# Kernel optimization log

Measured on AMD Instinct MI355X. Metric: run time of the kernel, lower is better.

The kernel has to match this reference:

```python
import jax, jax.numpy as jnp
import numpy as np

N_NODES = 100000
N_EDGES = 1600000
F_IN = 128
H = 32
N_CLASSES = 2
N_GRAPHS = 1000
BN_EPS = 1e-5


def _glorot(key, shape):
    fan_in, fan_out = shape
    lim = float(np.sqrt(6.0 / (fan_in + fan_out)))
    return jax.random.uniform(key, shape, jnp.float32, -lim, lim)


def setup_inputs() -> dict:
    key = jax.random.key(0)
    ks = jax.random.split(key, 16)
    x = jax.random.normal(ks[0], (N_NODES, F_IN), jnp.float32)
    edge_index = jax.random.randint(ks[1], (2, N_EDGES), 0, N_NODES, jnp.int64)
    batch = jnp.sort(jax.random.randint(ks[2], (N_NODES,), 0, N_GRAPHS, jnp.int64))
    return {
        "x": x,
        "edge_index": edge_index,
        "batch": batch,
        # GIN layer 1 MLP: Linear(F_IN,H) -> BN(H) -> ReLU -> Linear(H,H)
        "W1": _glorot(ks[3], (F_IN, H)), "b1": jnp.zeros((H,), jnp.float32),
        "g1": jnp.ones((H,), jnp.float32), "be1": jnp.zeros((H,), jnp.float32),
        "W2": _glorot(ks[4], (H, H)), "b2": jnp.zeros((H,), jnp.float32),
        # GIN layer 2 MLP
        "W3": _glorot(ks[5], (H, H)), "b3": jnp.zeros((H,), jnp.float32),
        "g2": jnp.ones((H,), jnp.float32), "be2": jnp.zeros((H,), jnp.float32),
        "W4": _glorot(ks[6], (H, H)), "b4": jnp.zeros((H,), jnp.float32),
        # classifier: Linear(2H,H) -> ReLU -> (Dropout eval) -> Linear(H,C)
        "Wc1": _glorot(ks[7], (2 * H, H)), "bc1": jnp.zeros((H,), jnp.float32),
        "Wc2": _glorot(ks[8], (H, N_CLASSES)), "bc2": jnp.zeros((N_CLASSES,), jnp.float32),
    }


def _gin_conv(x, src, dst, W_a, b_a, g, be, W_b, b_b):
    # GIN aggregation with eps=0: (1+eps)*x + sum_{j in N(i)} x_j
    agg = x + jax.ops.segment_sum(x[src], dst, num_segments=N_NODES)
    h = agg @ W_a + b_a                    # [N, H]
    # BatchNorm1d over node dim (training-mode batch stats)
    mu = jnp.mean(h, axis=0)
    var = jnp.var(h, axis=0)
    h = (h - mu) * jax.lax.rsqrt(var + BN_EPS) * g + be
    h = jax.nn.relu(h)
    return h @ W_b + b_b                   # [N, H]


def reference(x, edge_index, batch,
              W1, b1, g1, be1, W2, b2,
              W3, b3, g2, be2, W4, b4,
              Wc1, bc1, Wc2, bc2):
    src, dst = edge_index[0], edge_index[1]
    h = jax.nn.relu(_gin_conv(x, src, dst, W1, b1, g1, be1, W2, b2))
    h = _gin_conv(h, src, dst, W3, b3, g2, be2, W4, b4)   # [N, H]
    # global mean + max pool per graph
    counts = jax.ops.segment_sum(jnp.ones((N_NODES,), h.dtype), batch,
                                 num_segments=N_GRAPHS)              # [G]
    sums = jax.ops.segment_sum(h, batch, num_segments=N_GRAPHS)      # [G, H]
    mean = sums / jnp.maximum(counts, 1.0)[:, None]
    mx = jax.ops.segment_max(h, batch, num_segments=N_GRAPHS)
    mx = jnp.where(counts[:, None] > 0, mx, 0.0)
    z = jnp.concatenate([mean, mx], axis=-1)                          # [G, 2H]
    z = jax.nn.relu(z @ Wc1 + bc1)                                    # dropout: eval mode (identity)
    return z @ Wc2 + bc2                                              # [G, C]
```

## Files before the change

### kernel.cpp

```cpp
#include <hip/hip_runtime.h>


#define H 32
#define FIN 128
#define AGG_BLOCKS 2048
#define BNRED_NB 64

#define BKT_SHIFT 9
#define BKT_SZ 512
#define ACHUNK 4096

__device__ __forceinline__ int lower_bound_i(const int* __restrict__ a, int n, int key) {
  int lo = 0, hi = n;
  while (lo < hi) { int mid = (lo + hi) >> 1; if (a[mid] < key) lo = mid + 1; else hi = mid; }
  return lo;
}


__global__ __launch_bounds__(256) void k_bhist(const int* __restrict__ dst, int E,
                                               int* __restrict__ gbcnt) {
  __shared__ int cnt[256];
  int t = threadIdx.x;
  int e0 = blockIdx.x * ACHUNK, e1 = min(e0 + ACHUNK, E);
  cnt[t] = 0;
  __syncthreads();
  for (int i = e0 + t; i < e1; i += 256) atomicAdd(&cnt[dst[i] >> BKT_SHIFT], 1);
  __syncthreads();
  if (cnt[t] > 0) atomicAdd(&gbcnt[t], cnt[t]);
}

__global__ __launch_bounds__(256) void k_bscan(const int* __restrict__ gbcnt, int nbuck,
                                               int* __restrict__ bbase, int* __restrict__ bcur) {
  int t = threadIdx.x;
  __shared__ int sh[256];
  int v0 = (t < nbuck) ? gbcnt[t] : 0;
  sh[t] = v0;
  __syncthreads();
  for (int d = 1; d < 256; d <<= 1) {
    int v = (t >= d) ? sh[t - d] : 0;
    __syncthreads();
    sh[t] += v;
    __syncthreads();
  }
  int excl = sh[t] - v0;
  if (t < nbuck) { bbase[t] = excl; bcur[t] = excl; }
  if (t == 255) bbase[nbuck] = sh[255];
}

__global__ __launch_bounds__(256) void k_bucketA(const int* __restrict__ src, const int* __restrict__ dst,
                                                 int E, int* __restrict__ bcur,
                                                 unsigned* __restrict__ staging) {
  __shared__ int cnt[256];
  __shared__ int base[256];
  int t = threadIdx.x;
  int e0 = blockIdx.x * ACHUNK, e1 = min(e0 + ACHUNK, E);
  cnt[t] = 0;
  __syncthreads();
  for (int i = e0 + t; i < e1; i += 256) atomicAdd(&cnt[dst[i] >> BKT_SHIFT], 1);
  __syncthreads();
  int c = cnt[t];
  base[t] = (c > 0) ? atomicAdd(&bcur[t], c) : 0;
  __syncthreads();
  for (int i = e0 + t; i < e1; i += 256) {
    int d = dst[i];
    int p = atomicAdd(&base[d >> BKT_SHIFT], 1);
    staging[p] = ((unsigned)(d & (BKT_SZ - 1)) << 17) | (unsigned)src[i];
  }
}

__global__ __launch_bounds__(256) void k_bucketB(const unsigned* __restrict__ staging,
                                                 const int* __restrict__ bbase, int N,
                                                 int* __restrict__ row_ptr, int* __restrict__ csr) {
  __shared__ int cnt[BKT_SZ];
  __shared__ int ptr[BKT_SZ];
  __shared__ int sc[256];
  int t = threadIdx.x, b = blockIdx.x;
  int nb0 = b << BKT_SHIFT;
  int nb1 = min(nb0 + BKT_SZ, N);
  int seg0 = bbase[b];
  int len = bbase[b + 1] - seg0;
  cnt[t] = 0; cnt[t + 256] = 0;
  __syncthreads();
  for (int i = t; i < len; i += 256) atomicAdd(&cnt[staging[seg0 + i] >> 17], 1);
  __syncthreads();
  int s2 = cnt[2 * t] + cnt[2 * t + 1];
  sc[t] = s2;
  __syncthreads();
  for (int d = 1; d < 256; d <<= 1) {
    int v = (t >= d) ? sc[t - d] : 0;
    __syncthreads();
    sc[t] += v;
    __syncthreads();
  }
  int base0 = sc[t] - s2;
  ptr[2 * t] = base0;
  ptr[2 * t + 1] = base0 + cnt[2 * t];
  __syncthreads();
  int nn = nb1 - nb0;
  if (2 * t < nn)     row_ptr[nb0 + 2 * t]     = seg0 + ptr[2 * t];
  if (2 * t + 1 < nn) row_ptr[nb0 + 2 * t + 1] = seg0 + ptr[2 * t + 1];
  if (t == 0 && nb1 == N) row_ptr[N] = seg0 + len;
  __syncthreads();
  for (int i = t; i < len; i += 256) {
    unsigned e = staging[seg0 + i];
    int d = (int)(e >> 17);
    int k = atomicAdd(&ptr[d], 1);
    csr[seg0 + k] = (int)(e & 0x1FFFFu);
  }
}


__global__ __launch_bounds__(256) void k_gemm1(const float* __restrict__ x, const float* __restrict__ W,
                                               float* __restrict__ y, int N) {
  __shared__ __align__(16) float ws[FIN * H];
  __shared__ __align__(16) float xs[128 * 33];
  int t = threadIdx.x;
  for (int i = t; i < FIN * H; i += 256) ws[i] = W[i];
  int nb = blockIdx.x * 128;
  int r0 = (t >> 3) * 4;
  int c0 = (t & 7) * 4;
  float acc[4][4] = {{0.f,0.f,0.f,0.f},{0.f,0.f,0.f,0.f},{0.f,0.f,0.f,0.f},{0.f,0.f,0.f,0.f}};
  for (int kb = 0; kb < FIN; kb += 32) {
    __syncthreads();
    for (int i = t; i < 1024; i += 256) {
      int n = i >> 3, k4 = (i & 7) * 4;
      float4 v = make_float4(0.f, 0.f, 0.f, 0.f);
      int gn = nb + n;
      if (gn < N) v = *(const float4*)&x[(size_t)gn * FIN + kb + k4];
      xs[n * 33 + k4 + 0] = v.x; xs[n * 33 + k4 + 1] = v.y;
      xs[n * 33 + k4 + 2] = v.z; xs[n * 33 + k4 + 3] = v.w;
    }
    __syncthreads();
#pragma unroll
    for (int k = 0; k < 32; ++k) {
      float4 wv = *(const float4*)&ws[(kb + k) * H + c0];
      float x0 = xs[(r0 + 0) * 33 + k];
      float x1 = xs[(r0 + 1) * 33 + k];
      float x2 = xs[(r0 + 2) * 33 + k];
      float x3 = xs[(r0 + 3) * 33 + k];
      acc[0][0] += x0 * wv.x; acc[0][1] += x0 * wv.y; acc[0][2] += x0 * wv.z; acc[0][3] += x0 * wv.w;
      acc[1][0] += x1 * wv.x; acc[1][1] += x1 * wv.y; acc[1][2] += x1 * wv.z; acc[1][3] += x1 * wv.w;
      acc[2][0] += x2 * wv.x; acc[2][1] += x2 * wv.y; acc[2][2] += x2 * wv.z; acc[2][3] += x2 * wv.w;
      acc[3][0] += x3 * wv.x; acc[3][1] += x3 * wv.y; acc[3][2] += x3 * wv.z; acc[3][3] += x3 * wv.w;
    }
  }
#pragma unroll
  for (int r = 0; r < 4; ++r) {
    int gn = nb + r0 + r;
    if (gn < N)
      *(float4*)&y[(size_t)gn * H + c0] = make_float4(acc[r][0], acc[r][1], acc[r][2], acc[r][3]);
  }
}

__global__ __launch_bounds__(256) void k_agg(const float* __restrict__ y, const float* __restrict__ bias,
                                             const int* __restrict__ row_ptr, const int* __restrict__ csr,
                                             float* __restrict__ hout, float* __restrict__ bn_part, int N) {
  int wid = threadIdx.x >> 6, lane = threadIdx.x & 63;
  int c = lane & 31, ep = lane >> 5;
  float rsum = 0.f, rsq = 0.f;
  float bc = bias[c];
  int stride = gridDim.x * 4;
  for (int n = blockIdx.x * 4 + wid; n < N; n += stride) {
    int beg = row_ptr[n], end = row_ptr[n + 1];
    float acc = 0.f;
    for (int b0 = beg; b0 < end; b0 += 64) {
      int m = end - b0; if (m > 64) m = 64;
      int idx = (lane < m) ? csr[b0 + lane] : 0;
      int r = 0;
      for (; r + 8 <= m; r += 8) {
        int j0 = __shfl(idx, r + 0 + ep, 64);
        int j1 = __shfl(idx, r + 2 + ep, 64);
        int j2 = __shfl(idx, r + 4 + ep, 64);
        int j3 = __shfl(idx, r + 6 + ep, 64);
        float v0 = y[(size_t)j0 * H + c];
        float v1 = y[(size_t)j1 * H + c];
        float v2 = y[(size_t)j2 * H + c];
        float v3 = y[(size_t)j3 * H + c];
        acc += (v0 + v1) + (v2 + v3);
      }
      for (; r < m; r += 2) {
        int s = r + ep;
        int j = __shfl(idx, (s < m) ? s : 0, 64);
        float val = y[(size_t)j * H + c];
        if (s < m) acc += val;
      }
    }
    acc += __shfl_xor(acc, 32, 64);
    float v = acc + y[(size_t)n * H + c] + bc;
    if (ep == 0) {
      hout[(size_t)n * H + c] = v;
      rsum += v; rsq += v * v;
    }
  }
  __shared__ float bsum[4][H], bsq[4][H];
  if (ep == 0) { bsum[wid][c] = rsum; bsq[wid][c] = rsq; }
  __syncthreads();
  if (threadIdx.x < H) {
    int cc = threadIdx.x;
    bn_part[(size_t)blockIdx.x * 64 + cc]     = bsum[0][cc] + bsum[1][cc] + bsum[2][cc] + bsum[3][cc];
    bn_part[(size_t)blockIdx.x * 64 + H + cc] = bsq[0][cc] + bsq[1][cc] + bsq[2][cc] + bsq[3][cc];
  }
}

__global__ __launch_bounds__(256) void k_bnred(const float* __restrict__ part,
                                               float* __restrict__ part2) {
  int t = threadIdx.x, b = blockIdx.x;
  int col = t & 63, q = t >> 6;
  int rpb = AGG_BLOCKS / BNRED_NB;
  int r0 = b * rpb + q * (rpb / 4);
  float s = 0.f;
  for (int r = r0; r < r0 + rpb / 4; ++r) s += part[(size_t)r * 64 + col];
  __shared__ float red[4][64];
  red[q][col] = s;
  __syncthreads();
  if (t < 64) part2[(size_t)b * 64 + t] = red[0][t] + red[1][t] + red[2][t] + red[3][t];
}

__global__ __launch_bounds__(256) void k_bnfin(const float* __restrict__ part, int nblk,
                                               const float* __restrict__ gma, const float* __restrict__ bet,
                                               float* __restrict__ sc, float invN) {
  int t = threadIdx.x;
  int col = t & 63, q = t >> 6;
  int per = nblk >> 2;
  float s = 0.f;
  for (int r = q * per; r < (q + 1) * per; ++r) s += part[(size_t)r * 64 + col];
  __shared__ float red[4][64];
  __shared__ float tot[64];
  red[q][col] = s;
  __syncthreads();
  if (t < 64) tot[t] = red[0][t] + red[1][t] + red[2][t] + red[3][t];
  __syncthreads();
  if (t < H) {
    float mean = tot[t] * invN;
    float var = tot[H + t] * invN - mean * mean;
    float scale = gma[t] * rsqrtf(var + 1e-5f);
    sc[t] = scale;
    sc[H + t] = bet[t] - mean * scale;
  }
}

__global__ __launch_bounds__(256) void k_mlp1(const float* __restrict__ h1, const float* __restrict__ sc,
                                              const float* __restrict__ W2, const float* __restrict__ b2,
                                              const float* __restrict__ W3, float* __restrict__ y2, int N) {
  __shared__ __align__(16) float ws2[H * H], ws3[H * H];
  int t = threadIdx.x;
  for (int i = t; i < H * H; i += 256) { ws2[i] = W2[i]; ws3[i] = W3[i]; }
  __syncthreads();
  int lane = t & 63, wid = t >> 6;
  int c = lane & 31;
  int n = (blockIdx.x * 4 + wid) * 2 + (lane >> 5);
  if (n >= N) return;
  float h = h1[(size_t)n * H + c];
  float a = fmaxf(h * sc[c] + sc[H + c], 0.f);
  float u = b2[c];
#pragma unroll
  for (int k = 0; k < H; ++k)
    u += __shfl(a, k, 32) * ws2[k * H + c];
  u = fmaxf(u, 0.f);
  float o = 0.f;
#pragma unroll
  for (int k = 0; k < H; ++k)
    o += __shfl(u, k, 32) * ws3[k * H + c];
  y2[(size_t)n * H + c] = o;
}

__global__ __launch_bounds__(256) void k_mlp2(const float* __restrict__ hpre, const float* __restrict__ sc,
                                              const float* __restrict__ W4, const float* __restrict__ b4,
                                              float* __restrict__ h2, int N) {
  __shared__ __align__(16) float ws4[H * H];
  int t = threadIdx.x;
  for (int i = t; i < H * H; i += 256) ws4[i] = W4[i];
  __syncthreads();
  int lane = t & 63, wid = t >> 6;
  int c = lane & 31;
  int n = (blockIdx.x * 4 + wid) * 2 + (lane >> 5);
  if (n >= N) return;
  float h = hpre[(size_t)n * H + c];
  float a = fmaxf(h * sc[c] + sc[H + c], 0.f);
  float o = b4[c];
#pragma unroll
  for (int k = 0; k < H; ++k)
    o += __shfl(a, k, 32) * ws4[k * H + c];
  h2[(size_t)n * H + c] = o;
}

__global__ __launch_bounds__(256) void k_pool(const float* __restrict__ h2, const int* __restrict__ batch,
                                              int N, int G, float* __restrict__ z) {
  int wid = threadIdx.x >> 6, lane = threadIdx.x & 63;
  int g = blockIdx.x * 4 + wid;
  if (g >= G) return;
  int beg = lower_bound_i(batch, N, g);
  int end = lower_bound_i(batch, N, g + 1);
  int c = lane & 31, ep = lane >> 5;
  float s = 0.f, m = -3.402823466e38f;
  for (int i = beg + ep; i < end; i += 2) {
    float v = h2[(size_t)i * H + c];
    s += v; m = fmaxf(m, v);
  }
  s += __shfl_xor(s, 32, 64);
  m = fmaxf(m, __shfl_xor(m, 32, 64));
  if (ep == 0) {
    int cnt = end - beg;
    z[(size_t)g * 64 + c]     = (cnt > 0) ? s / (float)cnt : 0.f;
    z[(size_t)g * 64 + H + c] = (cnt > 0) ? m : 0.f;
  }
}

__global__ __launch_bounds__(256) void k_cls(const float* __restrict__ z, const float* __restrict__ Wc1,
                                             const float* __restrict__ bc1, const float* __restrict__ Wc2,
                                             const float* __restrict__ bc2, float* __restrict__ out, int G) {
  __shared__ __align__(16) float w1s[64 * H];
  __shared__ float w2s[H * 2], b1s[H], b2s[2];
  int t = threadIdx.x;
  for (int i = t; i < 64 * H; i += 256) w1s[i] = Wc1[i];
  if (t < H * 2) w2s[t] = Wc2[t];
  if (t < H) b1s[t] = bc1[t];
  if (t < 2) b2s[t] = bc2[t];
  __syncthreads();
  int g = blockIdx.x * 256 + t;
  if (g >= G) return;
  float zr[64], u[H];
  const float4* zp = (const float4*)&z[(size_t)g * 64];
#pragma unroll
  for (int q = 0; q < 16; ++q) {
    float4 v = zp[q];
    zr[q * 4 + 0] = v.x; zr[q * 4 + 1] = v.y; zr[q * 4 + 2] = v.z; zr[q * 4 + 3] = v.w;
  }
#pragma unroll
  for (int c = 0; c < H; ++c) u[c] = b1s[c];
#pragma unroll
  for (int k = 0; k < 64; ++k) {
    float av = zr[k];
    const float4* wr = (const float4*)&w1s[k * H];
#pragma unroll
    for (int q = 0; q < H / 4; ++q) {
      float4 wv = wr[q];
      u[q * 4 + 0] += av * wv.x; u[q * 4 + 1] += av * wv.y;
      u[q * 4 + 2] += av * wv.z; u[q * 4 + 3] += av * wv.w;
    }
  }
  float o0 = b2s[0], o1 = b2s[1];
#pragma unroll
  for (int k = 0; k < H; ++k) {
    float uv = fmaxf(u[k], 0.f);
    o0 += uv * w2s[k * 2 + 0];
    o1 += uv * w2s[k * 2 + 1];
  }
  out[(size_t)g * 2 + 0] = o0;
  out[(size_t)g * 2 + 1] = o1;
}

extern "C" void kernel_launch(void* const* d_in, const int* in_sizes, int n_in,
                              void* d_out, int out_size, void* d_ws, size_t ws_size,
                              hipStream_t stream) {
  const float* x    = (const float*)d_in[0];
  const int*   eidx = (const int*)d_in[1];
  const int*   batch= (const int*)d_in[2];
  const float* W1 = (const float*)d_in[3];
  const float* b1 = (const float*)d_in[4];
  const float* g1 = (const float*)d_in[5];
  const float* be1= (const float*)d_in[6];
  const float* W2 = (const float*)d_in[7];
  const float* b2 = (const float*)d_in[8];
  const float* W3 = (const float*)d_in[9];
  const float* b3 = (const float*)d_in[10];
  const float* g2 = (const float*)d_in[11];
  const float* be2= (const float*)d_in[12];
  const float* W4 = (const float*)d_in[13];
  const float* b4 = (const float*)d_in[14];
  const float* Wc1= (const float*)d_in[15];
  const float* bc1= (const float*)d_in[16];
  const float* Wc2= (const float*)d_in[17];
  const float* bc2= (const float*)d_in[18];
  (void)n_in; (void)ws_size;

  int N = in_sizes[2];
  int E = in_sizes[1] / 2;
  int G = out_size / 2;
  int nbuck = (N + BKT_SZ - 1) >> BKT_SHIFT;
  const int* srcv = eidx;
  const int* dstv = eidx + E;

  char* w = (char*)d_ws;
  auto carve = [&](size_t bytes) { void* p = (void*)w; w += (bytes + 255) & ~(size_t)255; return p; };
  float*    bufA    = (float*)carve((size_t)N * H * 4);
  float*    bufB    = (float*)carve((size_t)N * H * 4);
  int*      row_ptr = (int*)carve((size_t)(N + 1) * 4);
  int*      csr     = (int*)carve((size_t)E * 4);
  unsigned* staging = (unsigned*)carve((size_t)E * 4);
  int*      gbcnt   = (int*)carve(256 * 4);
  int*      bbase   = (int*)carve(257 * 4);
  int*      bcur    = (int*)carve(256 * 4);
  float*    bnp     = (float*)carve((size_t)AGG_BLOCKS * 64 * 4);
  float*    bnp2    = (float*)carve((size_t)BNRED_NB * 64 * 4);
  float*    sc1     = (float*)carve(64 * 4);
  float*    sc2     = (float*)carve(64 * 4);
  float*    z       = (float*)carve((size_t)G * 64 * 4);

  int abk = (E + ACHUNK - 1) / ACHUNK;
  int mlpblk = ((N + 1) / 2 + 3) / 4;

  hipMemsetAsync(gbcnt, 0, 256 * 4, stream);
  k_bhist<<<abk, 256, 0, stream>>>(dstv, E, gbcnt);
  k_bscan<<<1, 256, 0, stream>>>(gbcnt, nbuck, bbase, bcur);
  k_bucketA<<<abk, 256, 0, stream>>>(srcv, dstv, E, bcur, staging);
  k_bucketB<<<nbuck, 256, 0, stream>>>(staging, bbase, N, row_ptr, csr);
  k_gemm1<<<(N + 127) / 128, 256, 0, stream>>>(x, W1, bufA, N);
  k_agg<<<AGG_BLOCKS, 256, 0, stream>>>(bufA, b1, row_ptr, csr, bufB, bnp, N);
  k_bnred<<<BNRED_NB, 256, 0, stream>>>(bnp, bnp2);
  k_bnfin<<<1, 256, 0, stream>>>(bnp2, BNRED_NB, g1, be1, sc1, 1.0f / (float)N);
  k_mlp1<<<mlpblk, 256, 0, stream>>>(bufB, sc1, W2, b2, W3, bufA, N);
  k_agg<<<AGG_BLOCKS, 256, 0, stream>>>(bufA, b3, row_ptr, csr, bufB, bnp, N);
  k_bnred<<<BNRED_NB, 256, 0, stream>>>(bnp, bnp2);
  k_bnfin<<<1, 256, 0, stream>>>(bnp2, BNRED_NB, g2, be2, sc2, 1.0f / (float)N);
  k_mlp2<<<mlpblk, 256, 0, stream>>>(bufB, sc2, W4, b4, bufA, N);
  k_pool<<<(G + 3) / 4, 256, 0, stream>>>(bufA, batch, N, G, z);
  k_cls<<<(G + 255) / 256, 256, 0, stream>>>(z, Wc1, bc1, Wc2, bc2, (float*)d_out, G);
}
```

Baseline: 413.8 us.

## Tile the per-node MLP kernels as 128-node register-blocked GEMMs in shared memory

k_mlp1 and k_mlp2 now stage a 128-node tile of activations in padded shared memory. Each thread computes a 4x4 register block using float4 weight loads, instead of one output per lane built from 32 shuffles. The goal is to cut shuffle and LDS instruction overhead and to use vectorized global loads and stores. The cost is more shared memory per block, which may lower occupancy, and extra barriers.

New measurement: 389.6 us. 5.9% less time.

```diff
diff --git a/kernel.cpp b/kernel.cpp
--- a/kernel.cpp
+++ b/kernel.cpp
@@ -243,45 +243,123 @@
                                               const float* __restrict__ W2, const float* __restrict__ b2,
                                               const float* __restrict__ W3, float* __restrict__ y2, int N) {
   __shared__ __align__(16) float ws2[H * H], ws3[H * H];
+  __shared__ __align__(16) float as[128 * 33];
+  __shared__ __align__(16) float us[128 * 33];
+  __shared__ float scs[2 * H], b2s[H];
   int t = threadIdx.x;
   for (int i = t; i < H * H; i += 256) { ws2[i] = W2[i]; ws3[i] = W3[i]; }
-  __syncthreads();
-  int lane = t & 63, wid = t >> 6;
-  int c = lane & 31;
-  int n = (blockIdx.x * 4 + wid) * 2 + (lane >> 5);
-  if (n >= N) return;
-  float h = h1[(size_t)n * H + c];
-  float a = fmaxf(h * sc[c] + sc[H + c], 0.f);
-  float u = b2[c];
-#pragma unroll
-  for (int k = 0; k < H; ++k)
-    u += __shfl(a, k, 32) * ws2[k * H + c];
-  u = fmaxf(u, 0.f);
-  float o = 0.f;
-#pragma unroll
-  for (int k = 0; k < H; ++k)
-    o += __shfl(u, k, 32) * ws3[k * H + c];
-  y2[(size_t)n * H + c] = o;
+  if (t < 2 * H) scs[t] = sc[t];
+  if (t < H) b2s[t] = b2[t];
+  __syncthreads();
+  int nb = blockIdx.x * 128;
+  for (int i = t; i < 1024; i += 256) {
+    int n = i >> 3, c4 = (i & 7) * 4;
+    int gn = nb + n;
+    float4 v = make_float4(0.f, 0.f, 0.f, 0.f);
+    if (gn < N) v = *(const float4*)&h1[(size_t)gn * H + c4];
+    as[n * 33 + c4 + 0] = fmaxf(v.x * scs[c4 + 0] + scs[H + c4 + 0], 0.f);
+    as[n * 33 + c4 + 1] = fmaxf(v.y * scs[c4 + 1] + scs[H + c4 + 1], 0.f);
+    as[n * 33 + c4 + 2] = fmaxf(v.z * scs[c4 + 2] + scs[H + c4 + 2], 0.f);
+    as[n * 33 + c4 + 3] = fmaxf(v.w * scs[c4 + 3] + scs[H + c4 + 3], 0.f);
+  }
+  __syncthreads();
+  int r0 = (t >> 3) * 4, c0 = (t & 7) * 4;
+  float acc[4][4];
+#pragma unroll
+  for (int i = 0; i < 4; ++i)
+#pragma unroll
+    for (int j = 0; j < 4; ++j) acc[i][j] = b2s[c0 + j];
+#pragma unroll
+  for (int k = 0; k < H; ++k) {
+    float4 wv = *(const float4*)&ws2[k * H + c0];
+    float x0 = as[(r0 + 0) * 33 + k];
+    float x1 = as[(r0 + 1) * 33 + k];
+    float x2 = as[(r0 + 2) * 33 + k];
+    float x3 = as[(r0 + 3) * 33 + k];
+    acc[0][0] += x0 * wv.x; acc[0][1] += x0 * wv.y; acc[0][2] += x0 * wv.z; acc[0][3] += x0 * wv.w;
+    acc[1][0] += x1 * wv.x; acc[1][1] += x1 * wv.y; acc[1][2] += x1 * wv.z; acc[1][3] += x1 * wv.w;
+    acc[2][0] += x2 * wv.x; acc[2][1] += x2 * wv.y; acc[2][2] += x2 * wv.z; acc[2][3] += x2 * wv.w;
+    acc[3][0] += x3 * wv.x; acc[3][1] += x3 * wv.y; acc[3][2] += x3 * wv.z; acc[3][3] += x3 * wv.w;
+  }
+#pragma unroll
+  for (int i = 0; i < 4; ++i) {
+    us[(r0 + i) * 33 + c0 + 0] = fmaxf(acc[i][0], 0.f);
+    us[(r0 + i) * 33 + c0 + 1] = fmaxf(acc[i][1], 0.f);
+    us[(r0 + i) * 33 + c0 + 2] = fmaxf(acc[i][2], 0.f);
+    us[(r0 + i) * 33 + c0 + 3] = fmaxf(acc[i][3], 0.f);
+  }
+  __syncthreads();
+#pragma unroll
+  for (int i = 0; i < 4; ++i)
+#pragma unroll
+    for (int j = 0; j < 4; ++j) acc[i][j] = 0.f;
+#pragma unroll
+  for (int k = 0; k < H; ++k) {
+    float4 wv = *(const float4*)&ws3[k * H + c0];
+    float x0 = us[(r0 + 0) * 33 + k];
+    float x1 = us[(r0 + 1) * 33 + k];
+    float x2 = us[(r0 + 2) * 33 + k];
+    float x3 = us[(r0 + 3) * 33 + k];
+    acc[0][0] += x0 * wv.x; acc[0][1] += x0 * wv.y; acc[0][2] += x0 * wv.z; acc[0][3] += x0 * wv.w;
+    acc[1][0] += x1 * wv.x; acc[1][1] += x1 * wv.y; acc[1][2] += x1 * wv.z; acc[1][3] += x1 * wv.w;
+    acc[2][0] += x2 * wv.x; acc[2][1] += x2 * wv.y; acc[2][2] += x2 * wv.z; acc[2][3] += x2 * wv.w;
+    acc[3][0] += x3 * wv.x; acc[3][1] += x3 * wv.y; acc[3][2] += x3 * wv.z; acc[3][3] += x3 * wv.w;
+  }
+#pragma unroll
+  for (int i = 0; i < 4; ++i) {
+    int gn = nb + r0 + i;
+    if (gn < N)
+      *(float4*)&y2[(size_t)gn * H + c0] = make_float4(acc[i][0], acc[i][1], acc[i][2], acc[i][3]);
+  }
 }
 
 __global__ __launch_bounds__(256) void k_mlp2(const float* __restrict__ hpre, const float* __restrict__ sc,
                                               const float* __restrict__ W4, const float* __restrict__ b4,
                                               float* __restrict__ h2, int N) {
   __shared__ __align__(16) float ws4[H * H];
+  __shared__ __align__(16) float as[128 * 33];
+  __shared__ float scs[2 * H], b4s[H];
   int t = threadIdx.x;
   for (int i = t; i < H * H; i += 256) ws4[i] = W4[i];
-  __syncthreads();
-  int lane = t & 63, wid = t >> 6;
-  int c = lane & 31;
-  int n = (blockIdx.x * 4 + wid) * 2 + (lane >> 5);
-  if (n >= N) return;
-  float h = hpre[(size_t)n * H + c];
-  float a = fmaxf(h * sc[c] + sc[H + c], 0.f);
-  float o = b4[c];
-#pragma unroll
-  for (int k = 0; k < H; ++k)
-    o += __shfl(a, k, 32) * ws4[k * H + c];
-  h2[(size_t)n * H + c] = o;
+  if (t < 2 * H) scs[t] = sc[t];
+  if (t < H) b4s[t] = b4[t];
+  __syncthreads();
+  int nb = blockIdx.x * 128;
+  for (int i = t; i < 1024; i += 256) {
+    int n = i >> 3, c4 = (i & 7) * 4;
+    int gn = nb + n;
+    float4 v = make_float4(0.f, 0.f, 0.f, 0.f);
+    if (gn < N) v = *(const float4*)&hpre[(size_t)gn * H + c4];
+    as[n * 33 + c4 + 0] = fmaxf(v.x * scs[c4 + 0] + scs[H + c4 + 0], 0.f);
+    as[n * 33 + c4 + 1] = fmaxf(v.y * scs[c4 + 1] + scs[H + c4 + 1], 0.f);
+    as[n * 33 + c4 + 2] = fmaxf(v.z * scs[c4 + 2] + scs[H + c4 + 2], 0.f);
+    as[n * 33 + c4 + 3] = fmaxf(v.w * scs[c4 + 3] + scs[H + c4 + 3], 0.f);
+  }
+  __syncthreads();
+  int r0 = (t >> 3) * 4, c0 = (t & 7) * 4;
+  float acc[4][4];
+#pragma unroll
+  for (int i = 0; i < 4; ++i)
+#pragma unroll
+    for (int j = 0; j < 4; ++j) acc[i][j] = b4s[c0 + j];
+#pragma unroll
+  for (int k = 0; k < H; ++k) {
+    float4 wv = *(const float4*)&ws4[k * H + c0];
+    float x0 = as[(r0 + 0) * 33 + k];
+    float x1 = as[(r0 + 1) * 33 + k];
+    float x2 = as[(r0 + 2) * 33 + k];
+    float x3 = as[(r0 + 3) * 33 + k];
+    acc[0][0] += x0 * wv.x; acc[0][1] += x0 * wv.y; acc[0][2] += x0 * wv.z; acc[0][3] += x0 * wv.w;
+    acc[1][0] += x1 * wv.x; acc[1][1] += x1 * wv.y; acc[1][2] += x1 * wv.z; acc[1][3] += x1 * wv.w;
+    acc[2][0] += x2 * wv.x; acc[2][1] += x2 * wv.y; acc[2][2] += x2 * wv.z; acc[2][3] += x2 * wv.w;
+    acc[3][0] += x3 * wv.x; acc[3][1] += x3 * wv.y; acc[3][2] += x3 * wv.z; acc[3][3] += x3 * wv.w;
+  }
+#pragma unroll
+  for (int i = 0; i < 4; ++i) {
+    int gn = nb + r0 + i;
+    if (gn < N)
+      *(float4*)&h2[(size_t)gn * H + c0] = make_float4(acc[i][0], acc[i][1], acc[i][2], acc[i][3]);
+  }
 }
 
 __global__ __launch_bounds__(256) void k_pool(const float* __restrict__ h2, const int* __restrict__ batch,
@@ -398,22 +476,22 @@
   float*    z       = (float*)carve((size_t)G * 64 * 4);
 
   int abk = (E + ACHUNK - 1) / ACHUNK;
-  int mlpblk = ((N + 1) / 2 + 3) / 4;
+  int tblk = (N + 127) / 128;
 
   hipMemsetAsync(gbcnt, 0, 256 * 4, stream);
   k_bhist<<<abk, 256, 0, stream>>>(dstv, E, gbcnt);
   k_bscan<<<1, 256, 0, stream>>>(gbcnt, nbuck, bbase, bcur);
   k_bucketA<<<abk, 256, 0, stream>>>(srcv, dstv, E, bcur, staging);
   k_bucketB<<<nbuck, 256, 0, stream>>>(staging, bbase, N, row_ptr, csr);
-  k_gemm1<<<(N + 127) / 128, 256, 0, stream>>>(x, W1, bufA, N);
+  k_gemm1<<<tblk, 256, 0, stream>>>(x, W1, bufA, N);
   k_agg<<<AGG_BLOCKS, 256, 0, stream>>>(bufA, b1, row_ptr, csr, bufB, bnp, N);
   k_bnred<<<BNRED_NB, 256, 0, stream>>>(bnp, bnp2);
   k_bnfin<<<1, 256, 0, stream>>>(bnp2, BNRED_NB, g1, be1, sc1, 1.0f / (float)N);
-  k_mlp1<<<mlpblk, 256, 0, stream>>>(bufB, sc1, W2, b2, W3, bufA, N);
+  k_mlp1<<<tblk, 256, 0, stream>>>(bufB, sc1, W2, b2, W3, bufA, N);
   k_agg<<<AGG_BLOCKS, 256, 0, stream>>>(bufA, b3, row_ptr, csr, bufB, bnp, N);
   k_bnred<<<BNRED_NB, 256, 0, stream>>>(bnp, bnp2);
   k_bnfin<<<1, 256, 0, stream>>>(bnp2, BNRED_NB, g2, be2, sc2, 1.0f / (float)N);
-  k_mlp2<<<mlpblk, 256, 0, stream>>>(bufB, sc2, W4, b4, bufA, N);
+  k_mlp2<<<tblk, 256, 0, stream>>>(bufB, sc2, W4, b4, bufA, N);
   k_pool<<<(G + 3) / 4, 256, 0, stream>>>(bufA, batch, N, G, z);
   k_cls<<<(G + 255) / 256, 256, 0, stream>>>(z, Wc1, bc1, Wc2, bc2, (float*)d_out, G);
 }
```
